# Kernel optimization log

Measured on AMD Instinct MI355X. Metric: run time of the kernel, lower is better.

Reference implementation:

```python
import jax, jax.numpy as jnp
import numpy as np

B, T, D = 2, 2048, 1024
H = 16
DH = D // H


def setup_inputs() -> dict:
    key = jax.random.key(0)
    ks = jax.random.split(key, 6)
    s = 1.0 / np.sqrt(D)
    return {
        "x": jax.random.normal(ks[0], (B, T, D), dtype=jnp.float32),
        "Wq": jax.random.normal(ks[1], (D, D), dtype=jnp.float32) * s,
        "Wk": jax.random.normal(ks[2], (D, D), dtype=jnp.float32) * s,
        "Wv": jax.random.normal(ks[3], (D, D), dtype=jnp.float32) * s,
        "Wo": jax.random.normal(ks[4], (D, D), dtype=jnp.float32) * s,
        "bo": jax.random.normal(ks[5], (D,), dtype=jnp.float32) * s,
    }


def reference(x, Wq, Wk, Wv, Wo, bo):
    b, t, _ = x.shape
    # separate Q/K/V projections (nn.Linear: x @ W.T, no bias)
    q = (x @ Wq.T).reshape(b, t, H, DH).transpose(0, 2, 1, 3)  # [b,h,t,hd]
    k = (x @ Wk.T).reshape(b, t, H, DH).transpose(0, 2, 1, 3)
    v = (x @ Wv.T).reshape(b, t, H, DH).transpose(0, 2, 1, 3)

    scores = jnp.einsum("bhqd,bhkd->bhqk", q, k)  # [b,h,t,t]
    causal = jnp.triu(jnp.ones((t, t), dtype=bool), k=1)
    scores = jnp.where(causal, -jnp.inf, scores)
    weights = jax.nn.softmax(scores / np.sqrt(DH), axis=-1)
    # dropout p=0.0 -> identity
    ctx = jnp.einsum("bhqk,bhkd->bhqd", weights, v)  # [b,h,t,hd]
    # NOTE: original code reshapes WITHOUT transposing heads back — replicate faithfully
    ctx = ctx.reshape(b, t, H * DH)
    return ctx @ Wo.T + bo
```

## Files before the change

### kernel.cpp

```cpp
#include <hip/hip_runtime.h>
#include <math.h>

#define BATCH 2
#define SEQ   2048
#define DIM   1024
#define NH    16
#define HD    64
#define MTOT  4096

typedef __attribute__((ext_vector_type(8)))  short bf16x8;
typedef __attribute__((ext_vector_type(4)))  float f32x4;
typedef __attribute__((ext_vector_type(16))) float f32x16;

__device__ __forceinline__ ushort f2bf(float f) {
    union { float f; unsigned u; } v; v.f = f;
    unsigned r = v.u + 0x7fffu + ((v.u >> 16) & 1u);
    return (ushort)(r >> 16);
}

__device__ __forceinline__ unsigned cvtpk_bf16(float lo, float hi) {
    unsigned r;
    asm("v_cvt_pk_bf16_f32 %0, %1, %2" : "=v"(r) : "v"(lo), "v"(hi));
    return r;
}

__global__ __launch_bounds__(256)
void cast_x_k(const float* __restrict__ s, ushort* __restrict__ d, int n4)
{
    for (int i = blockIdx.x * blockDim.x + threadIdx.x; i < n4;
         i += gridDim.x * blockDim.x) {
        float4 v = ((const float4*)s)[i];
        ushort4 o;
        o.x = f2bf(v.x); o.y = f2bf(v.y); o.z = f2bf(v.z); o.w = f2bf(v.w);
        ((ushort4*)d)[i] = o;
    }
}

__global__ __launch_bounds__(256)
void cast_w_k(const float* __restrict__ s0, const float* __restrict__ s1,
              const float* __restrict__ s2, const float* __restrict__ s3,
              ushort* __restrict__ d0, ushort* __restrict__ d1,
              ushort* __restrict__ d2, ushort* __restrict__ d3, int n4)
{
    const float* s = (blockIdx.y == 0) ? s0 : (blockIdx.y == 1) ? s1
                   : (blockIdx.y == 2) ? s2 : s3;
    ushort* d = (blockIdx.y == 0) ? d0 : (blockIdx.y == 1) ? d1
              : (blockIdx.y == 2) ? d2 : d3;
    for (int i = blockIdx.x * blockDim.x + threadIdx.x; i < n4;
         i += gridDim.x * blockDim.x) {
        float4 v = ((const float4*)s)[i];
        ushort4 o;
        o.x = f2bf(v.x); o.y = f2bf(v.y); o.z = f2bf(v.z); o.w = f2bf(v.w);
        ((ushort4*)d)[i] = o;
    }
}

template<int MODE>
__global__ __launch_bounds__(256)
void gemm_bf16(const ushort* __restrict__ A,
               const ushort* __restrict__ W0, const ushort* __restrict__ W1,
               const ushort* __restrict__ W2,
               ushort* __restrict__ D0, ushort* __restrict__ D1,
               ushort* __restrict__ D2,
               const float* __restrict__ bias, float* __restrict__ Fout)
{
    __shared__ __align__(16) ushort As[2][128 * 64];
    __shared__ __align__(16) ushort Bs[2][128 * 64];

    const int tid = threadIdx.x;
    const int w = tid >> 6, l = tid & 63;
    const int g = l >> 4, l15 = l & 15;
    const int wr = w >> 1, wc = w & 1;
    const int brow = blockIdx.x * 128, bcol = blockIdx.y * 128;

    const ushort* W = (MODE == 1) ? W0
                    : (blockIdx.z == 0 ? W0 : (blockIdx.z == 1 ? W1 : W2));
    ushort* Dst = (MODE == 1) ? (ushort*)0
                : (blockIdx.z == 0 ? D0 : (blockIdx.z == 1 ? D1 : D2));

    const int rsub = l >> 3;
    const int gc   = ((l & 7) ^ rsub) * 8;
    const size_t arow0 = (size_t)(brow + 32 * w + rsub) * DIM;
    const size_t brow0 = (size_t)(bcol + 32 * w + rsub) * DIM;

    auto STAGE = [&](int buf, int ktel) {
        #pragma unroll
        for (int i = 0; i < 4; ++i) {
            __builtin_amdgcn_global_load_lds(
                (const __attribute__((address_space(1))) void*)
                    &A[arow0 + (size_t)(8 * i) * DIM + ktel + gc],
                (__attribute__((address_space(3))) void*)
                    &As[buf][(32 * w + 8 * i) * 64], 16, 0, 0);
            __builtin_amdgcn_global_load_lds(
                (const __attribute__((address_space(1))) void*)
                    &W[brow0 + (size_t)(8 * i) * DIM + ktel + gc],
                (__attribute__((address_space(3))) void*)
                    &Bs[buf][(32 * w + 8 * i) * 64], 16, 0, 0);
        }
    };

    STAGE(0, 0);
    STAGE(1, 64);

    f32x4 acc[4][4] = {};

    for (int t = 0; t < 16; ++t) {
        const int cur = t & 1;
        if (t < 15) asm volatile("s_waitcnt vmcnt(8)" ::: "memory");
        else        asm volatile("s_waitcnt vmcnt(0)" ::: "memory");
        __builtin_amdgcn_s_barrier();
        __builtin_amdgcn_sched_barrier(0);

        #pragma unroll
        for (int kh = 0; kh < 2; ++kh) {
            bf16x8 af[4], bfr[4];
            #pragma unroll
            for (int mi = 0; mi < 4; ++mi) {
                int row = 64 * wr + 16 * mi + l15;
                af[mi] = *(const bf16x8*)&As[cur][row * 64 + (((4 * kh + g) ^ (row & 7)) * 8)];
            }
            #pragma unroll
            for (int nj = 0; nj < 4; ++nj) {
                int row = 64 * wc + 16 * nj + l15;
                bfr[nj] = *(const bf16x8*)&Bs[cur][row * 64 + (((4 * kh + g) ^ (row & 7)) * 8)];
            }
            __builtin_amdgcn_s_setprio(1);
            #pragma unroll
            for (int mi = 0; mi < 4; ++mi)
                #pragma unroll
                for (int nj = 0; nj < 4; ++nj)
                    acc[mi][nj] = __builtin_amdgcn_mfma_f32_16x16x32_bf16(
                        af[mi], bfr[nj], acc[mi][nj], 0, 0, 0);
            __builtin_amdgcn_s_setprio(0);
        }

        __builtin_amdgcn_sched_barrier(0);
        __builtin_amdgcn_s_barrier();
        if (t + 2 < 16) STAGE(cur, (t + 2) * 64);
    }

    if (MODE == 0) {
        const float osc = (blockIdx.z == 0) ? 0.125f : 1.0f;
        if (blockIdx.z == 2) {
            #pragma unroll
            for (int mi = 0; mi < 4; ++mi)
                #pragma unroll
                for (int nj = 0; nj < 4; ++nj)
                    #pragma unroll
                    for (int reg = 0; reg < 4; ++reg) {
                        int row = brow + 64 * wr + 16 * mi + 4 * g + reg;
                        int col = bcol + 64 * wc + 16 * nj + l15;
                        int b = row >> 11, t = row & (SEQ - 1);
                        int hh = col >> 6, hd = col & 63;
                        Dst[(size_t)(b * NH + hh) * SEQ * HD
                            + ((size_t)(t >> 3) * 64 + hd) * 8 + (t & 7)] =
                            f2bf(acc[mi][nj][reg]);
                    }
        } else {
            #pragma unroll
            for (int mi = 0; mi < 4; ++mi)
                #pragma unroll
                for (int nj = 0; nj < 4; ++nj)
                    #pragma unroll
                    for (int reg = 0; reg < 4; ++reg) {
                        int row = brow + 64 * wr + 16 * mi + 4 * g + reg;
                        int col = bcol + 64 * wc + 16 * nj + l15;
                        int b = row >> 11, t = row & (SEQ - 1);
                        int hh = col >> 6, hd = col & 63;
                        Dst[(size_t)(b * NH + hh) * SEQ * HD
                            + (((size_t)(t >> 5) * 8 + (hd >> 3)) * 32 + (t & 31)) * 8
                            + (hd & 7)] = f2bf(acc[mi][nj][reg] * osc);
                    }
        }
    } else {
        #pragma unroll
        for (int nj = 0; nj < 4; ++nj) {
            int col = bcol + 64 * wc + 16 * nj + l15;
            float bv = bias[col];
            #pragma unroll
            for (int mi = 0; mi < 4; ++mi)
                #pragma unroll
                for (int reg = 0; reg < 4; ++reg) {
                    int row = brow + 64 * wr + 16 * mi + 4 * g + reg;
                    Fout[(size_t)row * DIM + col] = acc[mi][nj][reg] + bv;
                }
        }
    }
}

__global__ __launch_bounds__(64, 2)
void attn_mfma4(const ushort* __restrict__ q, const ushort* __restrict__ k,
                const ushort* __restrict__ vt, ushort* __restrict__ ctx)
{
    __shared__ __align__(16) ushort Ob[32 * 64];

    const int l = threadIdx.x;
    const int l31 = l & 31, h = l >> 5;
    const int bh = blockIdx.y;
    const int qt = ((int)blockIdx.x + 7 * bh) & 63;
    const int qlo = qt * 32;
    const int last = qt >> 1;
    const float LOG2E = 1.44269504f;

    const ushort* Qg = q  + (size_t)bh * SEQ * HD;
    const ushort* Kg = k  + (size_t)bh * SEQ * HD;
    const ushort* Vg = vt + (size_t)bh * SEQ * HD;

    bf16x8 qf[4];
    #pragma unroll
    for (int s = 0; s < 4; ++s)
        qf[s] = *(const bf16x8*)&Qg[(((size_t)qt * 8 + 2 * s + h) * 32 + l31) * 8];

    f32x16 o[2] = {};
    float m = -3.0e38f, lsum = 0.f;

    bf16x8 kfA[8], kfB[8];
    #pragma unroll
    for (int s = 0; s < 4; ++s)
        #pragma unroll
        for (int f = 0; f < 2; ++f)
            kfA[2 * s + f] = *(const bf16x8*)
                &Kg[(((size_t)f * 8 + 2 * s + h) * 32 + l31) * 8];

    auto body = [&](bf16x8 (&kc)[8], bf16x8 (&kn)[8], int kt) {
        const int kvb = 64 * kt;

        bf16x8 vf[8];
        #pragma unroll
        for (int s4 = 0; s4 < 4; ++s4)
            #pragma unroll
            for (int dt = 0; dt < 2; ++dt)
                vf[2 * s4 + dt] = *(const bf16x8*)
                    &Vg[(((size_t)(8 * kt + 2 * s4 + h)) * 64 + 32 * dt + l31) * 8];

        f32x16 st[2] = {};
        #pragma unroll
        for (int s = 0; s < 4; ++s)
            #pragma unroll
            for (int f = 0; f < 2; ++f)
                st[f] = __builtin_amdgcn_mfma_f32_32x32x16_bf16(
                    kc[2 * s + f], qf[s], st[f], 0, 0, 0);

        if (kt < last) {
            #pragma unroll
            for (int s = 0; s < 4; ++s)
                #pragma unroll
                for (int f = 0; f < 2; ++f)
                    kn[2 * s + f] = *(const bf16x8*)
                        &Kg[(((size_t)(2 * kt + 2 + f) * 8 + 2 * s + h) * 32 + l31) * 8];
        }

        const int qg = qlo + l31;
        if (kvb + 63 > qlo) {
            #pragma unroll
            for (int f = 0; f < 2; ++f)
                #pragma unroll
                for (int r = 0; r < 16; ++r) {
                    int kvg = kvb + 32 * f + (r & 3) + 8 * (r >> 2) + 4 * h;
                    if (kvg > qg) st[f][r] = -INFINITY;
                }
        }

        float mx[8];
        #pragma unroll
        for (int i2 = 0; i2 < 8; ++i2) {
            const int f = i2 >> 2, rb = 4 * (i2 & 3);
            mx[i2] = fmaxf(fmaxf(st[f][rb], st[f][rb + 1]),
                           fmaxf(st[f][rb + 2], st[f][rb + 3]));
        }
        float tmax = fmaxf(fmaxf(fmaxf(mx[0], mx[1]), fmaxf(mx[2], mx[3])),
                           fmaxf(fmaxf(mx[4], mx[5]), fmaxf(mx[6], mx[7])));
        tmax = fmaxf(tmax, __shfl_xor(tmax, 32));
        float ty = fmaxf(tmax * LOG2E, -3.0e38f);

        if (!__all(ty - m <= 8.0f)) {
            float mn = fmaxf(m, ty);
            float sc = exp2f(m - mn);
            lsum *= sc;
            #pragma unroll
            for (int dt = 0; dt < 2; ++dt)
                #pragma unroll
                for (int r = 0; r < 16; ++r) o[dt][r] *= sc;
            m = mn;
        }

        float ls0 = 0.f, ls1 = 0.f, ls2 = 0.f, ls3 = 0.f;
        #pragma unroll
        for (int f = 0; f < 2; ++f)
            #pragma unroll
            for (int r = 0; r < 16; ++r) {
                float pv = exp2f(fmaf(st[f][r], LOG2E, -m));
                st[f][r] = pv;
                if ((r & 3) == 0) ls0 += pv;
                else if ((r & 3) == 1) ls1 += pv;
                else if ((r & 3) == 2) ls2 += pv;
                else ls3 += pv;
            }
        lsum += (ls0 + ls1) + (ls2 + ls3);

        #pragma unroll
        for (int s4 = 0; s4 < 4; ++s4) {
            const int f = s4 >> 1, rb2 = 8 * (s4 & 1);
            unsigned Aa = cvtpk_bf16(st[f][rb2 + 0], st[f][rb2 + 1]);
            unsigned Bb = cvtpk_bf16(st[f][rb2 + 2], st[f][rb2 + 3]);
            unsigned Cc = cvtpk_bf16(st[f][rb2 + 4], st[f][rb2 + 5]);
            unsigned Dd = cvtpk_bf16(st[f][rb2 + 6], st[f][rb2 + 7]);
            unsigned Ax = (unsigned)__shfl_xor((int)Aa, 32);
            unsigned Bx = (unsigned)__shfl_xor((int)Bb, 32);
            unsigned Cx = (unsigned)__shfl_xor((int)Cc, 32);
            unsigned Dx = (unsigned)__shfl_xor((int)Dd, 32);
            union { unsigned wv[4]; bf16x8 v; } pu;
            pu.wv[0] = h ? Cx : Aa;
            pu.wv[1] = h ? Dx : Bb;
            pu.wv[2] = h ? Cc : Ax;
            pu.wv[3] = h ? Dd : Bx;
            #pragma unroll
            for (int dt = 0; dt < 2; ++dt)
                o[dt] = __builtin_amdgcn_mfma_f32_32x32x16_bf16(
                    vf[2 * s4 + dt], pu.v, o[dt], 0, 0, 0);
        }
    };

    int kt = 0;
    while (true) {
        body(kfA, kfB, kt);
        if (++kt > last) break;
        body(kfB, kfA, kt);
        if (++kt > last) break;
    }

    float lt = lsum + __shfl_xor(lsum, 32);
    float inv = 1.0f / lt;

    #pragma unroll
    for (int dt = 0; dt < 2; ++dt)
        #pragma unroll
        for (int r = 0; r < 16; r += 2) {
            int d = 32 * dt + (r & 3) + 8 * (r >> 2) + 4 * h;
            unsigned wrd = cvtpk_bf16(o[dt][r] * inv, o[dt][r + 1] * inv);
            *(unsigned*)&Ob[l31 * 64 + (((d >> 3) ^ (l31 & 7)) * 8) + (d & 7)] = wrd;
        }
    asm volatile("s_waitcnt lgkmcnt(0)" ::: "memory");
    __builtin_amdgcn_sched_barrier(0);

    ushort* Cg = ctx + (size_t)bh * SEQ * HD + (size_t)qlo * HD;
    #pragma unroll
    for (int i = 0; i < 4; ++i) {
        int qq = l >> 1, c = (l & 1) * 4 + i;
        int4 vvv = *(const int4*)&Ob[qq * 64 + ((c ^ (qq & 7)) * 8)];
        *(int4*)&Cg[qq * 64 + c * 8] = vvv;
    }
}

extern "C" void kernel_launch(void* const* d_in, const int* in_sizes, int n_in,
                              void* d_out, int out_size, void* d_ws, size_t ws_size,
                              hipStream_t stream)
{
    (void)in_sizes; (void)n_in; (void)out_size; (void)ws_size;
    const float* x  = (const float*)d_in[0];
    const float* Wq = (const float*)d_in[1];
    const float* Wk = (const float*)d_in[2];
    const float* Wv = (const float*)d_in[3];
    const float* Wo = (const float*)d_in[4];
    const float* bo = (const float*)d_in[5];
    float* out = (float*)d_out;

    ushort* wsu  = (ushort*)d_ws;
    ushort* xb   = wsu;
    ushort* wqb  = wsu + 4194304;
    ushort* wkb  = wsu + 5242880;
    ushort* wvb  = wsu + 6291456;
    ushort* wob  = wsu + 7340032;
    ushort* qbuf = wsu + 8388608;
    ushort* kbuf = wsu + 12582912;
    ushort* vtb  = wsu + 16777216;
    ushort* ctxb = wsu + 20971520;

    cast_x_k<<<2048, 256, 0, stream>>>(x, xb, MTOT * DIM / 4);
    cast_w_k<<<dim3(512, 4), 256, 0, stream>>>(Wq, Wk, Wv, Wo,
                                               wqb, wkb, wvb, wob, DIM * DIM / 4);

    dim3 gqkv(MTOT / 128, DIM / 128, 3);
    gemm_bf16<0><<<gqkv, 256, 0, stream>>>(xb, wqb, wkb, wvb,
                                           qbuf, kbuf, vtb, nullptr, nullptr);

    dim3 ga(SEQ / 32, BATCH * NH);
    attn_mfma4<<<ga, 64, 0, stream>>>(qbuf, kbuf, vtb, ctxb);

    dim3 go(MTOT / 128, DIM / 128, 1);
    gemm_bf16<1><<<go, 256, 0, stream>>>(ctxb, wob, nullptr, nullptr,
                                         nullptr, nullptr, nullptr, bo, out);
}
```

Baseline: 124.1 us.

## Prefetch V fragments one tile ahead, schedule heavy query tiles first, merge casts

The attention kernel now double-buffers V fragments the same way as K, loading the next tile's V while the current tile is computed, so V global loads are no longer issued and awaited inside each iteration. The grid is reordered so the longest causal query tiles launch first (a longest-first order), in place of the old hashed permutation. The two cast kernels are merged into one launch covering x and all four weights. Costs are higher VGPR pressure from the extra V buffers, which may limit occupancy under launch_bounds(64,2), and an imbalanced cast grid where the x slice does four times the work of each weight slice.

```diff
diff --git a/kernel.cpp b/kernel.cpp
--- a/kernel.cpp
+++ b/kernel.cpp
@@ -25,27 +25,20 @@
 }
 
 __global__ __launch_bounds__(256)
-void cast_x_k(const float* __restrict__ s, ushort* __restrict__ d, int n4)
+void cast_all(const float* __restrict__ x,
+              const float* __restrict__ Wq, const float* __restrict__ Wk,
+              const float* __restrict__ Wv, const float* __restrict__ Wo,
+              ushort* __restrict__ xb,
+              ushort* __restrict__ wqb, ushort* __restrict__ wkb,
+              ushort* __restrict__ wvb, ushort* __restrict__ wob)
 {
-    for (int i = blockIdx.x * blockDim.x + threadIdx.x; i < n4;
-         i += gridDim.x * blockDim.x) {
-        float4 v = ((const float4*)s)[i];
-        ushort4 o;
-        o.x = f2bf(v.x); o.y = f2bf(v.y); o.z = f2bf(v.z); o.w = f2bf(v.w);
-        ((ushort4*)d)[i] = o;
-    }
-}
-
-__global__ __launch_bounds__(256)
-void cast_w_k(const float* __restrict__ s0, const float* __restrict__ s1,
-              const float* __restrict__ s2, const float* __restrict__ s3,
-              ushort* __restrict__ d0, ushort* __restrict__ d1,
-              ushort* __restrict__ d2, ushort* __restrict__ d3, int n4)
-{
-    const float* s = (blockIdx.y == 0) ? s0 : (blockIdx.y == 1) ? s1
-                   : (blockIdx.y == 2) ? s2 : s3;
-    ushort* d = (blockIdx.y == 0) ? d0 : (blockIdx.y == 1) ? d1
-              : (blockIdx.y == 2) ? d2 : d3;
+    const int z = blockIdx.y;
+    const float* s; ushort* d; int n4;
+    if (z == 0)      { s = x;  d = xb;  n4 = MTOT * DIM / 4; }
+    else if (z == 1) { s = Wq; d = wqb; n4 = DIM * DIM / 4; }
+    else if (z == 2) { s = Wk; d = wkb; n4 = DIM * DIM / 4; }
+    else if (z == 3) { s = Wv; d = wvb; n4 = DIM * DIM / 4; }
+    else             { s = Wo; d = wob; n4 = DIM * DIM / 4; }
     for (int i = blockIdx.x * blockDim.x + threadIdx.x; i < n4;
          i += gridDim.x * blockDim.x) {
         float4 v = ((const float4*)s)[i];
@@ -189,15 +182,15 @@
 }
 
 __global__ __launch_bounds__(64, 2)
-void attn_mfma4(const ushort* __restrict__ q, const ushort* __restrict__ k,
+void attn_mfma5(const ushort* __restrict__ q, const ushort* __restrict__ k,
                 const ushort* __restrict__ vt, ushort* __restrict__ ctx)
 {
     __shared__ __align__(16) ushort Ob[32 * 64];
 
     const int l = threadIdx.x;
     const int l31 = l & 31, h = l >> 5;
-    const int bh = blockIdx.y;
-    const int qt = ((int)blockIdx.x + 7 * bh) & 63;
+    const int bh = blockIdx.x;
+    const int qt = 63 - (int)blockIdx.y;
     const int qlo = qt * 32;
     const int last = qt >> 1;
     const float LOG2E = 1.44269504f;
@@ -214,24 +207,23 @@
     f32x16 o[2] = {};
     float m = -3.0e38f, lsum = 0.f;
 
-    bf16x8 kfA[8], kfB[8];
+    bf16x8 kfA[8], kfB[8], vfA[8], vfB[8];
     #pragma unroll
     for (int s = 0; s < 4; ++s)
         #pragma unroll
         for (int f = 0; f < 2; ++f)
             kfA[2 * s + f] = *(const bf16x8*)
                 &Kg[(((size_t)f * 8 + 2 * s + h) * 32 + l31) * 8];
-
-    auto body = [&](bf16x8 (&kc)[8], bf16x8 (&kn)[8], int kt) {
+    #pragma unroll
+    for (int s4 = 0; s4 < 4; ++s4)
+        #pragma unroll
+        for (int dt = 0; dt < 2; ++dt)
+            vfA[2 * s4 + dt] = *(const bf16x8*)
+                &Vg[(((size_t)(2 * s4 + h)) * 64 + 32 * dt + l31) * 8];
+
+    auto body = [&](bf16x8 (&kc)[8], bf16x8 (&kn)[8],
+                    bf16x8 (&vc)[8], bf16x8 (&vn)[8], int kt) {
         const int kvb = 64 * kt;
-
-        bf16x8 vf[8];
-        #pragma unroll
-        for (int s4 = 0; s4 < 4; ++s4)
-            #pragma unroll
-            for (int dt = 0; dt < 2; ++dt)
-                vf[2 * s4 + dt] = *(const bf16x8*)
-                    &Vg[(((size_t)(8 * kt + 2 * s4 + h)) * 64 + 32 * dt + l31) * 8];
 
         f32x16 st[2] = {};
         #pragma unroll
@@ -248,6 +240,12 @@
                 for (int f = 0; f < 2; ++f)
                     kn[2 * s + f] = *(const bf16x8*)
                         &Kg[(((size_t)(2 * kt + 2 + f) * 8 + 2 * s + h) * 32 + l31) * 8];
+            #pragma unroll
+            for (int s4 = 0; s4 < 4; ++s4)
+                #pragma unroll
+                for (int dt = 0; dt < 2; ++dt)
+                    vn[2 * s4 + dt] = *(const bf16x8*)
+                        &Vg[(((size_t)(8 * kt + 8 + 2 * s4 + h)) * 64 + 32 * dt + l31) * 8];
         }
 
         const int qg = qlo + l31;
@@ -317,15 +315,15 @@
             #pragma unroll
             for (int dt = 0; dt < 2; ++dt)
                 o[dt] = __builtin_amdgcn_mfma_f32_32x32x16_bf16(
-                    vf[2 * s4 + dt], pu.v, o[dt], 0, 0, 0);
+                    vc[2 * s4 + dt], pu.v, o[dt], 0, 0, 0);
         }
     };
 
     int kt = 0;
     while (true) {
-        body(kfA, kfB, kt);
+        body(kfA, kfB, vfA, vfB, kt);
         if (++kt > last) break;
-        body(kfB, kfA, kt);
+        body(kfB, kfA, vfB, vfA, kt);
         if (++kt > last) break;
     }
 
@@ -376,16 +374,15 @@
     ushort* vtb  = wsu + 16777216;
     ushort* ctxb = wsu + 20971520;
 
-    cast_x_k<<<2048, 256, 0, stream>>>(x, xb, MTOT * DIM / 4);
-    cast_w_k<<<dim3(512, 4), 256, 0, stream>>>(Wq, Wk, Wv, Wo,
-                                               wqb, wkb, wvb, wob, DIM * DIM / 4);
+    cast_all<<<dim3(512, 5), 256, 0, stream>>>(x, Wq, Wk, Wv, Wo,
+                                               xb, wqb, wkb, wvb, wob);
 
     dim3 gqkv(MTOT / 128, DIM / 128, 3);
     gemm_bf16<0><<<gqkv, 256, 0, stream>>>(xb, wqb, wkb, wvb,
                                            qbuf, kbuf, vtb, nullptr, nullptr);
 
-    dim3 ga(SEQ / 32, BATCH * NH);
-    attn_mfma4<<<ga, 64, 0, stream>>>(qbuf, kbuf, vtb, ctxb);
+    dim3 ga(BATCH * NH, SEQ / 32);
+    attn_mfma5<<<ga, 64, 0, stream>>>(qbuf, kbuf, vtb, ctxb);
 
     dim3 go(MTOT / 128, DIM / 128, 1);
     gemm_bf16<1><<<go, 256, 0, stream>>>(ctxb, wob, nullptr, nullptr,
```

After: 116.3 us. 6.2% less time.
